# Performance work log

Measured on AMD Instinct MI355X. Metric: run time of the kernel, lower is better.

The kernel has to match this reference:

```python
import jax, jax.numpy as jnp
import numpy as np

B, T, I, H, NL, O = 256, 512, 64, 256, 2, 4


def _lstm_layer(x, Wih, Whh, bih, bhh):
    # x: [B, T, I_in]; Wih: [4H, I_in]; Whh: [4H, H]; biases: [4H]
    # PyTorch gate order: i, f, g, o
    xg = jnp.einsum('bti,gi->btg', x, Wih) + (bih + bhh)  # [B, T, 4H]
    h0 = jnp.zeros((x.shape[0], Whh.shape[1]), x.dtype)
    c0 = jnp.zeros_like(h0)

    def step(carry, xg_t):
        h, c = carry
        g = xg_t + h @ Whh.T
        i, f, gg, o = jnp.split(g, 4, axis=-1)
        c = jax.nn.sigmoid(f) * c + jax.nn.sigmoid(i) * jnp.tanh(gg)
        h = jax.nn.sigmoid(o) * jnp.tanh(c)
        return (h, c), h

    (_, _), hs = jax.lax.scan(step, (h0, c0), jnp.swapaxes(xg, 0, 1))  # [T, B, H]
    return jnp.swapaxes(hs, 0, 1)  # [B, T, H]


def setup_inputs() -> dict:
    key = jax.random.key(0)
    ks = jax.random.split(key, 16)
    s = 1.0 / np.sqrt(H)
    u = lambda k, shape: jax.random.uniform(k, shape, jnp.float32, -s, s)
    return {
        'x': jax.random.normal(ks[0], (B, T, I), jnp.float32),
        'Wih0': u(ks[1], (4 * H, I)),
        'Whh0': u(ks[2], (4 * H, H)),
        'bih0': u(ks[3], (4 * H,)),
        'bhh0': u(ks[4], (4 * H,)),
        'Wih1': u(ks[5], (4 * H, H)),
        'Whh1': u(ks[6], (4 * H, H)),
        'bih1': u(ks[7], (4 * H,)),
        'bhh1': u(ks[8], (4 * H,)),
        'W1': u(ks[9], (5 * H, H)),
        'b1': u(ks[10], (5 * H,)),
        'W2': u(ks[11], (O, 5 * H)),
        'b2': u(ks[12], (O,)),
    }


def reference(x, Wih0, Whh0, bih0, bhh0, Wih1, Whh1, bih1, bhh1, W1, b1, W2, b2):
    h1 = _lstm_layer(x, Wih0, Whh0, bih0, bhh0)   # [B, T, H]
    h2 = _lstm_layer(h1, Wih1, Whh1, bih1, bhh1)  # [B, T, H]
    last = h2[:, -1, :]                            # [B, H]
    y = last @ W1.T + b1                           # [B, 5H]
    y = y @ W2.T + b2                              # [B, O]
    return y
```

## Files before the change

### kernel.cpp

```cpp
#include <hip/hip_runtime.h>
#include <stdint.h>

typedef unsigned short u16;
typedef unsigned int   u32;
typedef unsigned long long u64;
typedef __bf16 bf16_t;
typedef bf16_t bf16x8 __attribute__((ext_vector_type(8)));
typedef float  f32x4  __attribute__((ext_vector_type(4)));
typedef int    i32x4  __attribute__((ext_vector_type(4)));

#define NSTEPS 512
#define SPIN_LIM  (1<<17)
#define RETRY_LIM (1<<13)

#define WS_RING1 0u
#define WS_RING2 1048576u
#define WS_PROG  2097152u
#define WS_TOTAL 2098176u

#define SMEM_BYTES (64*520*2)

__device__ __forceinline__ u16 f2bf(float f) {
  u32 u = __float_as_uint(f);
  return (u16)((u + 0x7fffu + ((u >> 16) & 1u)) >> 16);
}
__device__ __forceinline__ float bf2f(u16 b) { return __uint_as_float(((u32)b) << 16); }
__device__ __forceinline__ float sigf(float x) { return 1.f / (1.f + __expf(-x)); }
__device__ __forceinline__ float tanhf_(float x) {
  float e = __expf(-2.f * fabsf(x));
  float t = (1.f - e) / (1.f + e);
  return x >= 0.f ? t : -t;
}

__device__ __forceinline__ void st_u32_sc1(u32* p, u32 v) {
  asm volatile("global_store_dword %0, %1, off sc1" :: "v"(p), "v"(v) : "memory");
}
__device__ __forceinline__ u64 ld_u64_sc1(const u64* p) {
  u64 v; asm volatile("global_load_dwordx2 %0, %1, off sc1\n\ts_waitcnt vmcnt(0)"
                      : "=v"(v) : "v"(p) : "memory"); return v;
}

#define LD16(hp)                                                           \
  asm volatile(                                                            \
    "global_load_dwordx4 %0,  %16, off sc1\n\t"                            \
    "global_load_dwordx4 %1,  %16, off offset:16 sc1\n\t"                  \
    "global_load_dwordx4 %2,  %16, off offset:128 sc1\n\t"                 \
    "global_load_dwordx4 %3,  %16, off offset:144 sc1\n\t"                 \
    "global_load_dwordx4 %4,  %16, off offset:256 sc1\n\t"                 \
    "global_load_dwordx4 %5,  %16, off offset:272 sc1\n\t"                 \
    "global_load_dwordx4 %6,  %16, off offset:384 sc1\n\t"                 \
    "global_load_dwordx4 %7,  %16, off offset:400 sc1\n\t"                 \
    "global_load_dwordx4 %8,  %16, off offset:512 sc1\n\t"                 \
    "global_load_dwordx4 %9,  %16, off offset:528 sc1\n\t"                 \
    "global_load_dwordx4 %10, %16, off offset:640 sc1\n\t"                 \
    "global_load_dwordx4 %11, %16, off offset:656 sc1\n\t"                 \
    "global_load_dwordx4 %12, %16, off offset:768 sc1\n\t"                 \
    "global_load_dwordx4 %13, %16, off offset:784 sc1\n\t"                 \
    "global_load_dwordx4 %14, %16, off offset:896 sc1\n\t"                 \
    "global_load_dwordx4 %15, %16, off offset:912 sc1\n\t"                 \
    "s_waitcnt vmcnt(0)"                                                   \
    : "=&v"(h[0]), "=&v"(h[1]), "=&v"(h[2]),  "=&v"(h[3]),                 \
      "=&v"(h[4]), "=&v"(h[5]), "=&v"(h[6]),  "=&v"(h[7]),                 \
      "=&v"(h[8]), "=&v"(h[9]), "=&v"(h[10]), "=&v"(h[11]),                \
      "=&v"(h[12]),"=&v"(h[13]),"=&v"(h[14]), "=&v"(h[15])                 \
    : "v"(hp) : "memory")

#define TAGPOLL(hp, want) do {                                             \
    u32 tb = ((u32)(want)) << 16; int it_ = 0;                             \
    for (;;) {                                                             \
      LD16(hp);                                                            \
      u32 bad = 0;                                                         \
      _Pragma("unroll")                                                    \
      for (int q_ = 0; q_ < 16; ++q_)                                      \
        bad |= ((u32)h[q_][0] ^ tb) | ((u32)h[q_][1] ^ tb)                 \
             | ((u32)h[q_][2] ^ tb) | ((u32)h[q_][3] ^ tb);                \
      bad &= 0xffff0000u;                                                  \
      if (__all(bad == 0)) break;                                          \
      if (++it_ > RETRY_LIM) break;                                        \
      __builtin_amdgcn_s_sleep(1);                                         \
    }                                                                      \
  } while (0)

__device__ __forceinline__ bf16x8 frag_from(i32x4 lo, i32x4 hi) {
  union { u32 w[4]; bf16x8 v; } u_;
  u_.w[0] = ((u32)lo[0] & 0xffffu) | ((u32)lo[1] << 16);
  u_.w[1] = ((u32)lo[2] & 0xffffu) | ((u32)lo[3] << 16);
  u_.w[2] = ((u32)hi[0] & 0xffffu) | ((u32)hi[1] << 16);
  u_.w[3] = ((u32)hi[2] & 0xffffu) | ((u32)hi[3] << 16);
  return u_.v;
}
__device__ __forceinline__ bf16x8 pack_bf8(float4 a, float4 b) {
  union { u32 w[4]; bf16x8 v; } u_;
  u_.w[0] = (u32)f2bf(a.x) | ((u32)f2bf(a.y) << 16);
  u_.w[1] = (u32)f2bf(a.z) | ((u32)f2bf(a.w) << 16);
  u_.w[2] = (u32)f2bf(b.x) | ((u32)f2bf(b.y) << 16);
  u_.w[3] = (u32)f2bf(b.z) | ((u32)f2bf(b.w) << 16);
  return u_.v;
}

__device__ __forceinline__ void spin64(const int* f, int lane, int target) {
  if (target <= 0) return;
  int it = 0;
  for (;;) {
    int v = __hip_atomic_load(&f[lane], __ATOMIC_RELAXED, __HIP_MEMORY_SCOPE_AGENT);
    if (__all(v >= target)) return;
    if (++it > SPIN_LIM) return;
    __builtin_amdgcn_s_sleep(2);
  }
}

__global__ void ws_init_kernel(int* p, int n) {
  int i = blockIdx.x * blockDim.x + threadIdx.x;
  if (i < n)
    __hip_atomic_store(&p[i], 0, __ATOMIC_RELAXED, __HIP_MEMORY_SCOPE_AGENT);
}

__global__ void __launch_bounds__(256)
lstm_persistent(const float* __restrict__ x,
                const float* __restrict__ Wih0, const float* __restrict__ Whh0,
                const float* __restrict__ bih0, const float* __restrict__ bhh0,
                const float* __restrict__ Wih1, const float* __restrict__ Whh1,
                const float* __restrict__ bih1, const float* __restrict__ bhh1,
                const float* __restrict__ W1, const float* __restrict__ b1,
                const float* __restrict__ W2, const float* __restrict__ b2,
                float* __restrict__ out, char* __restrict__ ws)
{
  extern __shared__ u16 smem[];
  const int tid  = threadIdx.x;
  const int lane = tid & 63;
  const int wv   = tid >> 6;
  const int n16  = lane & 15;
  const int quad = lane >> 4;
  const int blk  = blockIdx.x;
  const int layer = blk >> 6;
  const int b    = blk & 63;
  const int bi   = b >> 4, j = b & 15;
  const int j16  = j * 16;
  const int rowg0 = bi * 64;
  const int widx = j*4 + wv;
  const int arow = wv*16 + n16;

  u32* r1g = (u32*)(ws + WS_RING1) + (size_t)bi * 4 * 16384;
  u32* r2g = (u32*)(ws + WS_RING2) + (size_t)bi * 4 * 16384;
  int* prg = (int*)(ws + WS_PROG) + bi * 64;

  float bg[4];
  #pragma unroll
  for (int nt = 0; nt < 4; ++nt) {
    int wrow = nt*256 + j16 + n16;
    bg[nt] = layer ? (bih1[wrow] + bhh1[wrow]) : (bih0[wrow] + bhh0[wrow]);
  }
  float cst[4] = {0.f,0.f,0.f,0.f};
  i32x4 h[16];

  if (layer == 0) {
    for (int i = 0; i < 20; ++i) {
      int u = tid + i*256;
      int lr = u / 80, c4 = u % 80;
      int wrow = (lr >> 4)*256 + j16 + (lr & 15);
      float4 v = (c4 < 16) ? *(const float4*)(Wih0 + (size_t)wrow*64 + c4*4)
                           : *(const float4*)(Whh0 + (size_t)wrow*256 + (c4-16)*4);
      u16* d = smem + lr*328 + c4*4;
      d[0]=f2bf(v.x); d[1]=f2bf(v.y); d[2]=f2bf(v.z); d[3]=f2bf(v.w);
    }
    __syncthreads();
    const u16* bP = smem + n16*328 + quad*8;

    for (int t = 0; t < NSTEPS; ++t) {
      const float* xp = x + ((size_t)(rowg0 + arow)*NSTEPS + t)*64 + quad*8;
      float4 xa = *(const float4*)(xp);
      float4 xb = *(const float4*)(xp + 4);
      float4 xc = *(const float4*)(xp + 32);
      float4 xd = *(const float4*)(xp + 36);
      spin64(prg, lane, t - 3);
      { const char* hp = (const char*)(r1g + ((t+3)&3)*16384) + arow*1024 + quad*32;
        TAGPOLL(hp, t); }
      bf16x8 a0 = pack_bf8(xa, xb), a1 = pack_bf8(xc, xd);
      f32x4 acc[4] = {{0,0,0,0},{0,0,0,0},{0,0,0,0},{0,0,0,0}};
      #pragma unroll
      for (int nt = 0; nt < 4; ++nt)
        acc[nt] = __builtin_amdgcn_mfma_f32_16x16x32_bf16(
            a0, *(const bf16x8*)(bP + nt*16*328), acc[nt], 0,0,0);
      #pragma unroll
      for (int nt = 0; nt < 4; ++nt)
        acc[nt] = __builtin_amdgcn_mfma_f32_16x16x32_bf16(
            a1, *(const bf16x8*)(bP + nt*16*328 + 32), acc[nt], 0,0,0);
      #pragma unroll
      for (int kc = 0; kc < 8; ++kc) {
        bf16x8 a = frag_from(h[2*kc], h[2*kc+1]);
        #pragma unroll
        for (int nt = 0; nt < 4; ++nt)
          acc[nt] = __builtin_amdgcn_mfma_f32_16x16x32_bf16(
              a, *(const bf16x8*)(bP + nt*16*328 + 64 + kc*32), acc[nt], 0,0,0);
      }
      u32 tag = ((u32)(t+1)) << 16;
      u32* dst = r1g + (t&3)*16384;
      #pragma unroll
      for (int r = 0; r < 4; ++r) {
        float gi = acc[0][r] + bg[0];
        float gf = acc[1][r] + bg[1];
        float gg = acc[2][r] + bg[2];
        float go = acc[3][r] + bg[3];
        float c  = sigf(gf)*cst[r] + sigf(gi)*tanhf_(gg);
        cst[r] = c;
        int rl = wv*16 + quad*4 + r;
        st_u32_sc1(dst + rl*256 + j16 + n16, tag | (u32)f2bf(sigf(go)*tanhf_(c)));
      }
    }
    return;
  }

  for (int i = 0; i < 32; ++i) {
    int u = tid + i*256;
    int lr = u >> 7, c4 = u & 127;
    int wrow = (lr >> 4)*256 + j16 + (lr & 15);
    float4 v = (c4 < 64) ? *(const float4*)(Wih1 + (size_t)wrow*256 + c4*4)
                         : *(const float4*)(Whh1 + (size_t)wrow*256 + (c4-64)*4);
    u16* d = smem + lr*520 + c4*4;
    d[0]=f2bf(v.x); d[1]=f2bf(v.y); d[2]=f2bf(v.z); d[3]=f2bf(v.w);
  }
  __syncthreads();
  const u16* bP = smem + n16*520 + quad*8;

  for (int t = 0; t < NSTEPS; ++t) {
    { const char* hp = (const char*)(r1g + (t&3)*16384) + arow*1024 + quad*32;
      TAGPOLL(hp, t+1); }
    if (lane == 0)
      __hip_atomic_store(&prg[widx], t+1, __ATOMIC_RELAXED, __HIP_MEMORY_SCOPE_AGENT);
    f32x4 acc[4] = {{0,0,0,0},{0,0,0,0},{0,0,0,0},{0,0,0,0}};
    #pragma unroll
    for (int kc = 0; kc < 8; ++kc) {
      bf16x8 a = frag_from(h[2*kc], h[2*kc+1]);
      #pragma unroll
      for (int nt = 0; nt < 4; ++nt)
        acc[nt] = __builtin_amdgcn_mfma_f32_16x16x32_bf16(
            a, *(const bf16x8*)(bP + nt*16*520 + kc*32), acc[nt], 0,0,0);
    }
    { const char* hp = (const char*)(r2g + ((t+3)&3)*16384) + arow*1024 + quad*32;
      TAGPOLL(hp, t); }
    #pragma unroll
    for (int kc = 0; kc < 8; ++kc) {
      bf16x8 a = frag_from(h[2*kc], h[2*kc+1]);
      #pragma unroll
      for (int nt = 0; nt < 4; ++nt)
        acc[nt] = __builtin_amdgcn_mfma_f32_16x16x32_bf16(
            a, *(const bf16x8*)(bP + nt*16*520 + 256 + kc*32), acc[nt], 0,0,0);
    }
    u32 tag = ((u32)(t+1)) << 16;
    u32* dst = r2g + (t&3)*16384;
    #pragma unroll
    for (int r = 0; r < 4; ++r) {
      float gi = acc[0][r] + bg[0];
      float gf = acc[1][r] + bg[1];
      float gg = acc[2][r] + bg[2];
      float go = acc[3][r] + bg[3];
      float c  = sigf(gf)*cst[r] + sigf(gi)*tanhf_(gg);
      cst[r] = c;
      int rl = wv*16 + quad*4 + r;
      st_u32_sc1(dst + rl*256 + j16 + n16, tag | (u32)f2bf(sigf(go)*tanhf_(c)));
    }
  }

  {
    float* lastsh = (float*)smem;
    float* y1sh   = lastsh + 1024;
    float* psum   = y1sh + 5120;
    __syncthreads();
    {
      int row = tid >> 6, c = tid & 63;
      int lr = (b & 15)*4 + row;
      #pragma unroll
      for (int rep = 0; rep < 2; ++rep) {
        int cc = c + rep*64;
        const u64* p = (const u64*)((const char*)(r2g + 3*16384) + lr*1024 + cc*8);
        u64 v = 0; int it = 0;
        for (;;) {
          v = ld_u64_sc1(p);
          if (((v >> 16) & 0xffffull) == 512 && (v >> 48) == 512) break;
          if (++it > RETRY_LIM) break;
          __builtin_amdgcn_s_sleep(1);
        }
        lastsh[row*256 + cc*2 + 0] = bf2f((u16)(v & 0xffffu));
        lastsh[row*256 + cc*2 + 1] = bf2f((u16)((v >> 32) & 0xffffu));
      }
    }
    __syncthreads();
    for (int i = 0; i < 5; ++i) {
      int m = tid + i*256;
      const float* wr = W1 + (size_t)m*256;
      float a0=0.f,a1=0.f,a2=0.f,a3=0.f;
      for (int k = 0; k < 256; ++k) {
        float w = wr[k];
        a0 += w*lastsh[k];     a1 += w*lastsh[256+k];
        a2 += w*lastsh[512+k]; a3 += w*lastsh[768+k];
      }
      float bb = b1[m];
      y1sh[m] = a0+bb; y1sh[1280+m] = a1+bb; y1sh[2560+m] = a2+bb; y1sh[3840+m] = a3+bb;
    }
    __syncthreads();
    if (tid < 64) {
      int row = tid >> 4, o = (tid >> 2) & 3, q = tid & 3;
      const float* w2r = W2 + (size_t)o*1280 + q*320;
      const float* yr  = y1sh + row*1280 + q*320;
      float s = 0.f;
      for (int m = 0; m < 320; ++m) s += w2r[m]*yr[m];
      psum[tid] = s;
    }
    __syncthreads();
    if (tid < 16) {
      int row = tid >> 2, o = tid & 3;
      out[(b*4 + row)*4 + o] = b2[o] + psum[tid*4+0] + psum[tid*4+1]
                                     + psum[tid*4+2] + psum[tid*4+3];
    }
  }
}

extern "C" void kernel_launch(void* const* d_in, const int* in_sizes, int n_in,
                              void* d_out, int out_size, void* d_ws, size_t ws_size,
                              hipStream_t stream) {
  (void)in_sizes; (void)n_in; (void)out_size; (void)ws_size;
  const float* x    = (const float*)d_in[0];
  const float* Wih0 = (const float*)d_in[1];
  const float* Whh0 = (const float*)d_in[2];
  const float* bih0 = (const float*)d_in[3];
  const float* bhh0 = (const float*)d_in[4];
  const float* Wih1 = (const float*)d_in[5];
  const float* Whh1 = (const float*)d_in[6];
  const float* bih1 = (const float*)d_in[7];
  const float* bhh1 = (const float*)d_in[8];
  const float* W1   = (const float*)d_in[9];
  const float* b1   = (const float*)d_in[10];
  const float* W2   = (const float*)d_in[11];
  const float* b2   = (const float*)d_in[12];
  float* out = (float*)d_out;
  char* ws   = (char*)d_ws;

  hipLaunchKernelGGL(ws_init_kernel, dim3((WS_TOTAL/4 + 255)/256), dim3(256),
                     0, stream, (int*)ws, (int)(WS_TOTAL/4));

  hipFuncSetAttribute((const void*)lstm_persistent,
                      hipFuncAttributeMaxDynamicSharedMemorySize, SMEM_BYTES);

  void* args[] = { (void*)&x, (void*)&Wih0, (void*)&Whh0, (void*)&bih0, (void*)&bhh0,
                   (void*)&Wih1, (void*)&Whh1, (void*)&bih1, (void*)&bhh1,
                   (void*)&W1, (void*)&b1, (void*)&W2, (void*)&b2,
                   (void*)&out, (void*)&ws };
  hipLaunchCooperativeKernel((const void*)lstm_persistent, dim3(128), dim3(256),
                             args, SMEM_BYTES, stream);
}
```

Measured before the change: 2.765 ms.

## Deepen layer-0 ring, throttle spin checks, and prefetch layer-1 input during poll

The layer-0 to layer-1 hidden-state ring grows from 4 to 8 slots, and the workspace offsets are moved to make room. Layer 0 now checks consumer progress only every fourth step, so it can run further ahead with fewer global spins. Layer 1 issues the load for the next step's layer-0 output before it polls its own recurrent ring. At the top of the next step it validates the prefetched tags and falls back to polling only if they are stale. The aim is to hide cross-layer handoff latency, at the cost of more workspace, extra registers for a second fragment buffer, and subtler memory-ordering assumptions.

```diff
diff --git a/kernel.cpp b/kernel.cpp
--- a/kernel.cpp
+++ b/kernel.cpp
@@ -14,9 +14,9 @@
 #define RETRY_LIM (1<<13)
 
 #define WS_RING1 0u
-#define WS_RING2 1048576u
-#define WS_PROG  2097152u
-#define WS_TOTAL 2098176u
+#define WS_RING2 2097152u
+#define WS_PROG  3145728u
+#define WS_TOTAL 3146752u
 
 #define SMEM_BYTES (64*520*2)
 
@@ -40,8 +40,7 @@
                       : "=v"(v) : "v"(p) : "memory"); return v;
 }
 
-#define LD16(hp)                                                           \
-  asm volatile(                                                            \
+#define LD16_BODY                                                          \
     "global_load_dwordx4 %0,  %16, off sc1\n\t"                            \
     "global_load_dwordx4 %1,  %16, off offset:16 sc1\n\t"                  \
     "global_load_dwordx4 %2,  %16, off offset:128 sc1\n\t"                 \
@@ -57,24 +56,37 @@
     "global_load_dwordx4 %12, %16, off offset:768 sc1\n\t"                 \
     "global_load_dwordx4 %13, %16, off offset:784 sc1\n\t"                 \
     "global_load_dwordx4 %14, %16, off offset:896 sc1\n\t"                 \
-    "global_load_dwordx4 %15, %16, off offset:912 sc1\n\t"                 \
-    "s_waitcnt vmcnt(0)"                                                   \
-    : "=&v"(h[0]), "=&v"(h[1]), "=&v"(h[2]),  "=&v"(h[3]),                 \
-      "=&v"(h[4]), "=&v"(h[5]), "=&v"(h[6]),  "=&v"(h[7]),                 \
-      "=&v"(h[8]), "=&v"(h[9]), "=&v"(h[10]), "=&v"(h[11]),                \
-      "=&v"(h[12]),"=&v"(h[13]),"=&v"(h[14]), "=&v"(h[15])                 \
-    : "v"(hp) : "memory")
-
-#define TAGPOLL(hp, want) do {                                             \
+    "global_load_dwordx4 %15, %16, off offset:912 sc1"
+#define LD16_OUTS(A)                                                       \
+      "=&v"(A[0]), "=&v"(A[1]), "=&v"(A[2]),  "=&v"(A[3]),                 \
+      "=&v"(A[4]), "=&v"(A[5]), "=&v"(A[6]),  "=&v"(A[7]),                 \
+      "=&v"(A[8]), "=&v"(A[9]), "=&v"(A[10]), "=&v"(A[11]),                \
+      "=&v"(A[12]),"=&v"(A[13]),"=&v"(A[14]), "=&v"(A[15])
+
+#define LD16_N(A, P) \
+  asm volatile(LD16_BODY : LD16_OUTS(A) : "v"(P) : "memory")
+#define LD16_W(A, P) \
+  asm volatile(LD16_BODY "\n\ts_waitcnt vmcnt(0)" : LD16_OUTS(A) : "v"(P) : "memory")
+
+#define HREVAL(A)                                                          \
+  asm volatile("s_waitcnt vmcnt(4)"                                        \
+    : "+v"(A[0]), "+v"(A[1]), "+v"(A[2]),  "+v"(A[3]),                     \
+      "+v"(A[4]), "+v"(A[5]), "+v"(A[6]),  "+v"(A[7]),                     \
+      "+v"(A[8]), "+v"(A[9]), "+v"(A[10]), "+v"(A[11]),                    \
+      "+v"(A[12]),"+v"(A[13]),"+v"(A[14]), "+v"(A[15]) :: "memory")
+
+#define TAGCHK(A, TB, BAD) do {                                            \
+    _Pragma("unroll")                                                      \
+    for (int q_ = 0; q_ < 16; ++q_)                                        \
+      BAD |= ((u32)A[q_][0] ^ TB) | ((u32)A[q_][1] ^ TB)                   \
+           | ((u32)A[q_][2] ^ TB) | ((u32)A[q_][3] ^ TB);                  \
+  } while (0)
+
+#define TAGPOLL(A, hp, want) do {                                          \
     u32 tb = ((u32)(want)) << 16; int it_ = 0;                             \
     for (;;) {                                                             \
-      LD16(hp);                                                            \
-      u32 bad = 0;                                                         \
-      _Pragma("unroll")                                                    \
-      for (int q_ = 0; q_ < 16; ++q_)                                      \
-        bad |= ((u32)h[q_][0] ^ tb) | ((u32)h[q_][1] ^ tb)                 \
-             | ((u32)h[q_][2] ^ tb) | ((u32)h[q_][3] ^ tb);                \
-      bad &= 0xffff0000u;                                                  \
+      LD16_W(A, hp);                                                       \
+      u32 bad = 0; TAGCHK(A, tb, bad); bad &= 0xffff0000u;                 \
       if (__all(bad == 0)) break;                                          \
       if (++it_ > RETRY_LIM) break;                                        \
       __builtin_amdgcn_s_sleep(1);                                         \
@@ -140,7 +152,7 @@
   const int widx = j*4 + wv;
   const int arow = wv*16 + n16;
 
-  u32* r1g = (u32*)(ws + WS_RING1) + (size_t)bi * 4 * 16384;
+  u32* r1g = (u32*)(ws + WS_RING1) + (size_t)bi * 8 * 16384;
   u32* r2g = (u32*)(ws + WS_RING2) + (size_t)bi * 4 * 16384;
   int* prg = (int*)(ws + WS_PROG) + bi * 64;
 
@@ -172,9 +184,10 @@
       float4 xb = *(const float4*)(xp + 4);
       float4 xc = *(const float4*)(xp + 32);
       float4 xd = *(const float4*)(xp + 36);
-      spin64(prg, lane, t - 3);
-      { const char* hp = (const char*)(r1g + ((t+3)&3)*16384) + arow*1024 + quad*32;
-        TAGPOLL(hp, t); }
+      if ((t & 3) == 0)
+        spin64(prg, lane, t - 4);
+      { const char* hp = (const char*)(r1g + ((t+7)&7)*16384) + arow*1024 + quad*32;
+        TAGPOLL(h, hp, t); }
       bf16x8 a0 = pack_bf8(xa, xb), a1 = pack_bf8(xc, xd);
       f32x4 acc[4] = {{0,0,0,0},{0,0,0,0},{0,0,0,0},{0,0,0,0}};
       #pragma unroll
@@ -194,7 +207,7 @@
               a, *(const bf16x8*)(bP + nt*16*328 + 64 + kc*32), acc[nt], 0,0,0);
       }
       u32 tag = ((u32)(t+1)) << 16;
-      u32* dst = r1g + (t&3)*16384;
+      u32* dst = r1g + (t&7)*16384;
       #pragma unroll
       for (int r = 0; r < 4; ++r) {
         float gi = acc[0][r] + bg[0];
@@ -221,10 +234,22 @@
   }
   __syncthreads();
   const u16* bP = smem + n16*520 + quad*8;
+  i32x4 g[16];
+
+  { const char* p1 = (const char*)(r1g) + arow*1024 + quad*32;
+    LD16_N(h, p1);
+    asm volatile("s_waitcnt vmcnt(0)" ::: "memory"); }
 
   for (int t = 0; t < NSTEPS; ++t) {
-    { const char* hp = (const char*)(r1g + (t&3)*16384) + arow*1024 + quad*32;
-      TAGPOLL(hp, t+1); }
+    {
+      HREVAL(h);
+      u32 tb = ((u32)(t+1)) << 16, bad = 0;
+      TAGCHK(h, tb, bad); bad &= 0xffff0000u;
+      if (!__all(bad == 0)) {
+        const char* p1 = (const char*)(r1g + (t&7)*16384) + arow*1024 + quad*32;
+        TAGPOLL(h, p1, t+1);
+      }
+    }
     if (lane == 0)
       __hip_atomic_store(&prg[widx], t+1, __ATOMIC_RELAXED, __HIP_MEMORY_SCOPE_AGENT);
     f32x4 acc[4] = {{0,0,0,0},{0,0,0,0},{0,0,0,0},{0,0,0,0}};
@@ -236,11 +261,13 @@
         acc[nt] = __builtin_amdgcn_mfma_f32_16x16x32_bf16(
             a, *(const bf16x8*)(bP + nt*16*520 + kc*32), acc[nt], 0,0,0);
     }
-    { const char* hp = (const char*)(r2g + ((t+3)&3)*16384) + arow*1024 + quad*32;
-      TAGPOLL(hp, t); }
+    { const char* p1n = (const char*)(r1g + ((t+1)&7)*16384) + arow*1024 + quad*32;
+      LD16_N(h, p1n); }
+    { const char* p2 = (const char*)(r2g + ((t+3)&3)*16384) + arow*1024 + quad*32;
+      TAGPOLL(g, p2, t); }
     #pragma unroll
     for (int kc = 0; kc < 8; ++kc) {
-      bf16x8 a = frag_from(h[2*kc], h[2*kc+1]);
+      bf16x8 a = frag_from(g[2*kc], g[2*kc+1]);
       #pragma unroll
       for (int nt = 0; nt < 4; ++nt)
         acc[nt] = __builtin_amdgcn_mfma_f32_16x16x32_bf16(
```

Result: slower. 2.831 ms (+2.4%).

## Publish LSTM states via atomic exchange, halve progress spins, separate layer-2 poll buffer

Applied to the files above, without the earlier changes.

Per-element state publishes switch from sc1 global stores to agent-scope relaxed atomic exchanges. The aim is to make writes visible to polling workgroups sooner. Layer 1 now checks layer 2's progress only on even steps, with slack relaxed from 3 to 2, which cuts spin overhead on the ring-buffer handshake. Layer 2 polls its own recurrent state into a separate register array, so the layer-1 input fragments are no longer overwritten. This costs extra VGPRs and atomic traffic, and it changes how the ring slots are protected.

```diff
diff --git a/kernel.cpp b/kernel.cpp
--- a/kernel.cpp
+++ b/kernel.cpp
@@ -32,15 +32,15 @@
   return x >= 0.f ? t : -t;
 }
 
-__device__ __forceinline__ void st_u32_sc1(u32* p, u32 v) {
-  asm volatile("global_store_dword %0, %1, off sc1" :: "v"(p), "v"(v) : "memory");
+__device__ __forceinline__ void pub_u32(u32* p, u32 v) {
+  (void)__hip_atomic_exchange(p, v, __ATOMIC_RELAXED, __HIP_MEMORY_SCOPE_AGENT);
 }
 __device__ __forceinline__ u64 ld_u64_sc1(const u64* p) {
   u64 v; asm volatile("global_load_dwordx2 %0, %1, off sc1\n\ts_waitcnt vmcnt(0)"
                       : "=v"(v) : "v"(p) : "memory"); return v;
 }
 
-#define LD16(hp)                                                           \
+#define LD16_W(A, P)                                                       \
   asm volatile(                                                            \
     "global_load_dwordx4 %0,  %16, off sc1\n\t"                            \
     "global_load_dwordx4 %1,  %16, off offset:16 sc1\n\t"                  \
@@ -59,22 +59,24 @@
     "global_load_dwordx4 %14, %16, off offset:896 sc1\n\t"                 \
     "global_load_dwordx4 %15, %16, off offset:912 sc1\n\t"                 \
     "s_waitcnt vmcnt(0)"                                                   \
-    : "=&v"(h[0]), "=&v"(h[1]), "=&v"(h[2]),  "=&v"(h[3]),                 \
-      "=&v"(h[4]), "=&v"(h[5]), "=&v"(h[6]),  "=&v"(h[7]),                 \
-      "=&v"(h[8]), "=&v"(h[9]), "=&v"(h[10]), "=&v"(h[11]),                \
-      "=&v"(h[12]),"=&v"(h[13]),"=&v"(h[14]), "=&v"(h[15])                 \
-    : "v"(hp) : "memory")
-
-#define TAGPOLL(hp, want) do {                                             \
+    : "=&v"(A[0]), "=&v"(A[1]), "=&v"(A[2]),  "=&v"(A[3]),                 \
+      "=&v"(A[4]), "=&v"(A[5]), "=&v"(A[6]),  "=&v"(A[7]),                 \
+      "=&v"(A[8]), "=&v"(A[9]), "=&v"(A[10]), "=&v"(A[11]),                \
+      "=&v"(A[12]),"=&v"(A[13]),"=&v"(A[14]), "=&v"(A[15])                 \
+    : "v"(P) : "memory")
+
+#define TAGCHK(A, TB, BAD) do {                                            \
+    _Pragma("unroll")                                                      \
+    for (int q_ = 0; q_ < 16; ++q_)                                        \
+      BAD |= ((u32)A[q_][0] ^ TB) | ((u32)A[q_][1] ^ TB)                   \
+           | ((u32)A[q_][2] ^ TB) | ((u32)A[q_][3] ^ TB);                  \
+  } while (0)
+
+#define TAGPOLL(A, hp, want) do {                                          \
     u32 tb = ((u32)(want)) << 16; int it_ = 0;                             \
     for (;;) {                                                             \
-      LD16(hp);                                                            \
-      u32 bad = 0;                                                         \
-      _Pragma("unroll")                                                    \
-      for (int q_ = 0; q_ < 16; ++q_)                                      \
-        bad |= ((u32)h[q_][0] ^ tb) | ((u32)h[q_][1] ^ tb)                 \
-             | ((u32)h[q_][2] ^ tb) | ((u32)h[q_][3] ^ tb);                \
-      bad &= 0xffff0000u;                                                  \
+      LD16_W(A, hp);                                                       \
+      u32 bad = 0; TAGCHK(A, tb, bad); bad &= 0xffff0000u;                 \
       if (__all(bad == 0)) break;                                          \
       if (++it_ > RETRY_LIM) break;                                        \
       __builtin_amdgcn_s_sleep(1);                                         \
@@ -172,9 +174,10 @@
       float4 xb = *(const float4*)(xp + 4);
       float4 xc = *(const float4*)(xp + 32);
       float4 xd = *(const float4*)(xp + 36);
-      spin64(prg, lane, t - 3);
+      if ((t & 1) == 0)
+        spin64(prg, lane, t - 2);
       { const char* hp = (const char*)(r1g + ((t+3)&3)*16384) + arow*1024 + quad*32;
-        TAGPOLL(hp, t); }
+        TAGPOLL(h, hp, t); }
       bf16x8 a0 = pack_bf8(xa, xb), a1 = pack_bf8(xc, xd);
       f32x4 acc[4] = {{0,0,0,0},{0,0,0,0},{0,0,0,0},{0,0,0,0}};
       #pragma unroll
@@ -204,7 +207,7 @@
         float c  = sigf(gf)*cst[r] + sigf(gi)*tanhf_(gg);
         cst[r] = c;
         int rl = wv*16 + quad*4 + r;
-        st_u32_sc1(dst + rl*256 + j16 + n16, tag | (u32)f2bf(sigf(go)*tanhf_(c)));
+        pub_u32(dst + rl*256 + j16 + n16, tag | (u32)f2bf(sigf(go)*tanhf_(c)));
       }
     }
     return;
@@ -221,10 +224,11 @@
   }
   __syncthreads();
   const u16* bP = smem + n16*520 + quad*8;
+  i32x4 g[16];
 
   for (int t = 0; t < NSTEPS; ++t) {
     { const char* hp = (const char*)(r1g + (t&3)*16384) + arow*1024 + quad*32;
-      TAGPOLL(hp, t+1); }
+      TAGPOLL(h, hp, t+1); }
     if (lane == 0)
       __hip_atomic_store(&prg[widx], t+1, __ATOMIC_RELAXED, __HIP_MEMORY_SCOPE_AGENT);
     f32x4 acc[4] = {{0,0,0,0},{0,0,0,0},{0,0,0,0},{0,0,0,0}};
@@ -237,10 +241,10 @@
             a, *(const bf16x8*)(bP + nt*16*520 + kc*32), acc[nt], 0,0,0);
     }
     { const char* hp = (const char*)(r2g + ((t+3)&3)*16384) + arow*1024 + quad*32;
-      TAGPOLL(hp, t); }
+      TAGPOLL(g, hp, t); }
     #pragma unroll
     for (int kc = 0; kc < 8; ++kc) {
-      bf16x8 a = frag_from(h[2*kc], h[2*kc+1]);
+      bf16x8 a = frag_from(g[2*kc], g[2*kc+1]);
       #pragma unroll
       for (int nt = 0; nt < 4; ++nt)
         acc[nt] = __builtin_amdgcn_mfma_f32_16x16x32_bf16(
@@ -257,7 +261,7 @@
       float c  = sigf(gf)*cst[r] + sigf(gi)*tanhf_(gg);
       cst[r] = c;
       int rl = wv*16 + quad*4 + r;
-      st_u32_sc1(dst + rl*256 + j16 + n16, tag | (u32)f2bf(sigf(go)*tanhf_(c)));
+      pub_u32(dst + rl*256 + j16 + n16, tag | (u32)f2bf(sigf(go)*tanhf_(c)));
     }
   }
 
```

Result: faster. 2.692 ms (-2.7%).
